# Kernel optimization log

Hardware: AMD Instinct MI355X
Metric: run time of the kernel (lower is better)

## Reference

```python
import jax, jax.numpy as jnp
import numpy as np

D_MODEL = 1024
D_STATE = 64
BATCH = 4
SEQ_L = 4096
LN_EPS = 1e-5


def setup_inputs() -> dict:
    key = jax.random.key(0)
    ks = jax.random.split(key, 8)
    u = jax.random.normal(ks[0], (BATCH, SEQ_L, D_MODEL), jnp.float32)
    # Parameters mirroring StateSpaceLayer._initialize_parameters
    A_log = jax.random.uniform(ks[1], (D_STATE,), jnp.float32, -2.0, -0.1)
    xav = float(np.sqrt(6.0 / (D_STATE + D_MODEL)))
    B = jax.random.uniform(ks[2], (D_STATE, D_MODEL), jnp.float32, -xav, xav) * 0.1
    C = jax.random.uniform(ks[3], (D_MODEL, D_STATE), jnp.float32, -xav, xav) * 0.1
    D = jnp.zeros((D_MODEL,), jnp.float32)
    delta = jax.random.uniform(ks[4], (D_MODEL,), jnp.float32, 0.001, 0.1)
    gamma = jnp.ones((D_MODEL,), jnp.float32)
    beta = jnp.zeros((D_MODEL,), jnp.float32)
    freq_align = jax.random.normal(ks[5], (D_MODEL,), jnp.float32)
    reward = jax.random.normal(ks[6], (D_MODEL,), jnp.float32)
    return dict(u=u, A_log=A_log, B=B, C=C, D=D, delta=delta,
                gamma=gamma, beta=beta, freq_align=freq_align, reward=reward)


def reference(u, A_log, B, C, D, delta, gamma, beta, freq_align, reward):
    b, L, d = u.shape
    A = -jnp.exp(A_log)                                   # [N]
    # --- convolution kernel: K[k] = C @ (A_bar[0])^k, A_bar[0] = exp(delta[0]*A) ---
    k_idx = jnp.arange(L, dtype=u.dtype)                  # [L]
    powers = jnp.exp(k_idx[:, None] * (delta[0] * A)[None, :])  # [L, N]
    K = jnp.einsum('ln,dn->ld', powers, C)                # [L, D]
    # --- FFT-based causal (circular, zero-padded) convolution ---
    fft_size = 1 << int(np.ceil(np.log2(2 * L)))
    u_fft = jnp.fft.fft(u, n=fft_size, axis=1)            # [B, F, D] complex
    K_fft = jnp.fft.fft(K, n=fft_size, axis=0)            # [F, D] complex
    y = jnp.fft.ifft(u_fft * K_fft[None], axis=1).real[:, :L, :]
    # --- D skip connection ---
    y = y + u * D
    # --- FFT-based learning signals: scale spectrum, add real 'reward' to every bin ---
    y_fft = jnp.fft.fft(y, axis=1)
    y = jnp.fft.ifft(y_fft * freq_align + reward, axis=1).real
    # --- LayerNorm (eval-mode dropout = identity) ---
    mean = y.mean(-1, keepdims=True)
    var = y.var(-1, keepdims=True)
    y = (y - mean) / jnp.sqrt(var + LN_EPS) * gamma + beta
    # --- final state update with mean timescale ---
    delta_mean = delta.mean()
    A_bar_s = jnp.exp(delta_mean * A)                     # [N]
    A_safe = A + 1e-8 * jnp.sign(A)
    B_bar = ((A_bar_s - 1.0) / A_safe)[:, None] * B       # [N, D]
    state = jnp.zeros((b, A.shape[0]), u.dtype)
    final_state = A_bar_s * state + jnp.einsum('nd,bd->bn', B_bar, u[:, -1, :])
    return (y, final_state)
```

## Files before the change

kernel.cpp:

```cpp
#include <hip/hip_runtime.h>
#include <math.h>

#define BATCH  4
#define SEQL   4096
#define DMODEL 1024
#define NSTATE 64
#define LN_EPS 1e-5f
#define TB     16

typedef unsigned short u16;
typedef float f32x2 __attribute__((ext_vector_type(2)));

__device__ __forceinline__ f32x2 fma2(f32x2 a, f32x2 b, f32x2 c) {
#if __has_builtin(__builtin_elementwise_fma)
    return __builtin_elementwise_fma(a, b, c);
#else
    f32x2 d; d.x = fmaf(a.x, b.x, c.x); d.y = fmaf(a.y, b.y, c.y); return d;
#endif
}

__device__ __forceinline__ u16 f2bf(float x) {
    unsigned int b = __float_as_uint(x);
    b += 0x7FFF + ((b >> 16) & 1);
    return (u16)(b >> 16);
}
__device__ __forceinline__ float bf2f(u16 h) {
    return __uint_as_float(((unsigned int)h) << 16);
}

__global__ __launch_bounds__(256) void k_local(const float* __restrict__ u,
                                               const float* __restrict__ A_log,
                                               const float* __restrict__ delta,
                                               u16* __restrict__ f,
                                               int NCH, int TCH) {
    __shared__ float r_lds[NSTATE];
    const int tid = threadIdx.x;
    const int w = tid >> 6, l = tid & 63;
    const int b   = blockIdx.x / (16 * NCH);
    const int rem = blockIdx.x % (16 * NCH);
    const int dt  = rem / NCH;
    const int j   = rem % NCH;
    const int n0  = w << 4;
    const int d   = (dt << 6) | l;

    if (tid < NSTATE) r_lds[tid] = expf(delta[0] * -expf(A_log[tid]));
    __syncthreads();

    f32x2 r2[8], s2[8];
#pragma unroll
    for (int p = 0; p < 8; ++p) {
        r2[p] = *(const f32x2*)&r_lds[n0 + 2 * p];
        s2[p] = (f32x2)(0.f, 0.f);
    }

    const float* ub = u + ((size_t)b * SEQL + (size_t)j * TCH) * DMODEL + d;
    for (int tb = 0; tb < TCH / TB; ++tb) {
        float ur[TB];
#pragma unroll
        for (int t = 0; t < TB; ++t)
            ur[t] = ub[(size_t)(tb * TB + t) * DMODEL];
#pragma unroll
        for (int q = 0; q < 4; ++q) {
            f32x2 sa = s2[2*q], sb = s2[2*q+1];
            const f32x2 ra = r2[2*q], rb = r2[2*q+1];
#pragma unroll
            for (int t = 0; t < TB; ++t) {
                f32x2 u2; u2.x = ur[t]; u2.y = ur[t];
                sa = fma2(ra, sa, u2);
                sb = fma2(rb, sb, u2);
            }
            s2[2*q] = sa; s2[2*q+1] = sb;
        }
    }
    u16* fb = f + (((size_t)b * NCH + j) * NSTATE + n0) * DMODEL + d;
#pragma unroll
    for (int p = 0; p < 8; ++p) {
        fb[(size_t)(2*p)     * DMODEL] = f2bf(s2[p].x);
        fb[(size_t)(2*p + 1) * DMODEL] = f2bf(s2[p].y);
    }
}

__global__ __launch_bounds__(256) void k_pass2(const float* __restrict__ A_log,
                                               const float* __restrict__ delta,
                                               u16* __restrict__ f,
                                               int NCH, int TCH) {
    const int tid = blockIdx.x * 256 + threadIdx.x;
    const int d = tid & (DMODEL - 1);
    const int n = (tid >> 10) & (NSTATE - 1);
    const int b = tid >> 16;
    const float A  = -expf(A_log[n]);
    const float rT = expf((float)TCH * delta[0] * A);
    float I = 0.f;
    u16* p = f + ((size_t)b * NCH * NSTATE + n) * DMODEL + d;
    const size_t stride = (size_t)NSTATE * DMODEL;
    for (int j = 0; j < NCH; ++j) {
        float tmp = bf2f(p[(size_t)j * stride]);
        p[(size_t)j * stride] = f2bf(I);
        I = fmaf(rT, I, tmp);
    }
}

__global__ __launch_bounds__(256) void k_replay(const float* __restrict__ u,
                                                const float* __restrict__ A_log,
                                                const float* __restrict__ C,
                                                const float* __restrict__ Dvec,
                                                const float* __restrict__ delta,
                                                const u16* __restrict__ I,
                                                const float* __restrict__ fal,
                                                const float* __restrict__ rw,
                                                float* __restrict__ z,
                                                int NCH, int TCH) {
    __shared__ float r_lds[NSTATE];
    __shared__ float part[4][TB][64];
    const int tid = threadIdx.x;
    const int w = tid >> 6, l = tid & 63;
    const int b   = blockIdx.x / (16 * NCH);
    const int rem = blockIdx.x % (16 * NCH);
    const int dt  = rem / NCH;
    const int j   = rem % NCH;
    const int n0  = w << 4;
    const int d   = (dt << 6) | l;

    if (tid < NSTATE) r_lds[tid] = expf(delta[0] * -expf(A_log[tid]));
    __syncthreads();

    const float fad = fal[d];
    f32x2 r2[8], c2[8], s2[8];
#pragma unroll
    for (int p = 0; p < 8; ++p)
        r2[p] = *(const f32x2*)&r_lds[n0 + 2 * p];
#pragma unroll
    for (int p = 0; p < 8; ++p) {
        c2[p].x = fad * C[(size_t)d * NSTATE + n0 + 2*p];
        c2[p].y = fad * C[(size_t)d * NSTATE + n0 + 2*p + 1];
    }
    const u16* Ib = I + (((size_t)b * NCH + j) * NSTATE + n0) * DMODEL + d;
#pragma unroll
    for (int p = 0; p < 8; ++p) {
        s2[p].x = bf2f(Ib[(size_t)(2*p)     * DMODEL]);
        s2[p].y = bf2f(Ib[(size_t)(2*p + 1) * DMODEL]);
    }

    const float Ddf = Dvec[d] * fad;
    const float rwd = rw[d];
    const float* ub = u + ((size_t)b * SEQL + (size_t)j * TCH) * DMODEL + d;
    float*       zb = z + ((size_t)b * SEQL + (size_t)j * TCH) * DMODEL + d;

    for (int tb = 0; tb < TCH / TB; ++tb) {
        float ur[TB];
        f32x2 zr2[TB];
#pragma unroll
        for (int t = 0; t < TB; ++t) {
            ur[t] = ub[(size_t)(tb * TB + t) * DMODEL];
            zr2[t] = (f32x2)(0.f, 0.f);
        }
#pragma unroll
        for (int q = 0; q < 4; ++q) {
            f32x2 sa = s2[2*q], sb = s2[2*q+1];
            const f32x2 ra = r2[2*q], rb = r2[2*q+1];
            const f32x2 ca = c2[2*q], cb = c2[2*q+1];
#pragma unroll
            for (int t = 0; t < TB; ++t) {
                f32x2 u2; u2.x = ur[t]; u2.y = ur[t];
                sa = fma2(ra, sa, u2);
                sb = fma2(rb, sb, u2);
                zr2[t] = fma2(ca, sa, zr2[t]);
                zr2[t] = fma2(cb, sb, zr2[t]);
            }
            s2[2*q] = sa; s2[2*q+1] = sb;
        }
#pragma unroll
        for (int t = 0; t < TB; ++t) {
            float v = zr2[t].x + zr2[t].y;
            if (w == 0) v = fmaf(Ddf, ur[t], v);
            part[w][t][l] = v;
        }
        __syncthreads();
#pragma unroll
        for (int k = 0; k < 4; ++k) {
            const int t = (w << 2) | k;
            float v = (part[0][t][l] + part[1][t][l]) +
                      (part[2][t][l] + part[3][t][l]);
            if (j == 0 && tb == 0 && t == 0) v += rwd;
            zb[(size_t)(tb * TB + t) * DMODEL] = v;
        }
        __syncthreads();
    }
}

__global__ __launch_bounds__(256) void k_ln(float* __restrict__ y,
                                            const float* __restrict__ gamma,
                                            const float* __restrict__ beta) {
    const int tid = threadIdx.x;
    float4* row = (float4*)(y + (size_t)blockIdx.x * DMODEL);
    float4 v = row[tid];
    float sum = v.x + v.y + v.z + v.w;
    float sq  = v.x*v.x + v.y*v.y + v.z*v.z + v.w*v.w;
#pragma unroll
    for (int off = 32; off > 0; off >>= 1) {
        sum += __shfl_down(sum, off, 64);
        sq  += __shfl_down(sq,  off, 64);
    }
    __shared__ float red[8];
    const int wave = tid >> 6, lane = tid & 63;
    if (lane == 0) { red[wave] = sum; red[4 + wave] = sq; }
    __syncthreads();
    sum = red[0] + red[1] + red[2] + red[3];
    sq  = red[4] + red[5] + red[6] + red[7];
    const float mean = sum * (1.f / DMODEL);
    const float var  = sq * (1.f / DMODEL) - mean * mean;
    const float inv  = 1.f / sqrtf(var + LN_EPS);
    const float4 g  = ((const float4*)gamma)[tid];
    const float4 bb = ((const float4*)beta)[tid];
    float4 o;
    o.x = (v.x - mean) * inv * g.x + bb.x;
    o.y = (v.y - mean) * inv * g.y + bb.y;
    o.z = (v.z - mean) * inv * g.z + bb.z;
    o.w = (v.w - mean) * inv * g.w + bb.w;
    row[tid] = o;
}

__global__ __launch_bounds__(256) void k_state(const float* __restrict__ u,
                                               const float* __restrict__ A_log,
                                               const float* __restrict__ B,
                                               const float* __restrict__ delta,
                                               float* __restrict__ out) {
    const int n = blockIdx.x & 63;
    const int b = blockIdx.x >> 6;
    const int tid = threadIdx.x;
    const float* ul = u + ((size_t)b * SEQL + (SEQL - 1)) * DMODEL;
    const float* Bn = B + (size_t)n * DMODEL;
    float dot = 0.f, dsum = 0.f;
    for (int dd = tid; dd < DMODEL; dd += 256) {
        dot = fmaf(Bn[dd], ul[dd], dot);
        dsum += delta[dd];
    }
#pragma unroll
    for (int off = 32; off > 0; off >>= 1) {
        dot  += __shfl_down(dot,  off, 64);
        dsum += __shfl_down(dsum, off, 64);
    }
    __shared__ float red[8];
    const int wave = tid >> 6, lane = tid & 63;
    if (lane == 0) { red[wave] = dot; red[4 + wave] = dsum; }
    __syncthreads();
    if (tid == 0) {
        dot  = red[0] + red[1] + red[2] + red[3];
        dsum = red[4] + red[5] + red[6] + red[7];
        const float dmean = dsum * (1.f / DMODEL);
        const float A = -expf(A_log[n]);
        const float Abar = expf(dmean * A);
        const float Asafe = A + (A >= 0.f ? 1e-8f : -1e-8f);
        out[blockIdx.x] = ((Abar - 1.f) / Asafe) * dot;
    }
}

extern "C" void kernel_launch(void* const* d_in, const int* in_sizes, int n_in,
                              void* d_out, int out_size, void* d_ws, size_t ws_size,
                              hipStream_t stream) {
    const float* u     = (const float*)d_in[0];
    const float* A_log = (const float*)d_in[1];
    const float* B     = (const float*)d_in[2];
    const float* C     = (const float*)d_in[3];
    const float* Dv    = (const float*)d_in[4];
    const float* delta = (const float*)d_in[5];
    const float* gamma = (const float*)d_in[6];
    const float* beta  = (const float*)d_in[7];
    const float* fal   = (const float*)d_in[8];
    const float* rw    = (const float*)d_in[9];

    float* y  = (float*)d_out;
    float* st = y + (size_t)BATCH * SEQL * DMODEL;
    u16* f    = (u16*)d_ws;

    int NCH = 32;
    while (NCH > 4 && (size_t)BATCH * NCH * NSTATE * DMODEL * sizeof(u16) > ws_size)
        NCH >>= 1;
    const int TCH = SEQL / NCH;
    const int nb = BATCH * 16 * NCH;

    hipLaunchKernelGGL(k_local, dim3(nb), dim3(256), 0, stream, u, A_log, delta, f, NCH, TCH);
    hipLaunchKernelGGL(k_pass2, dim3(BATCH * NSTATE * DMODEL / 256), dim3(256), 0, stream,
                       A_log, delta, f, NCH, TCH);
    hipLaunchKernelGGL(k_replay, dim3(nb), dim3(256), 0, stream,
                       u, A_log, C, Dv, delta, f, fal, rw, y, NCH, TCH);
    hipLaunchKernelGGL(k_ln, dim3(BATCH * SEQL), dim3(256), 0, stream, y, gamma, beta);
    hipLaunchKernelGGL(k_state, dim3(BATCH * NSTATE), dim3(256), 0, stream,
                       u, A_log, B, delta, st);
}
```

Measured before the change: 130.8 us.

## Store replay output as bf16 intermediate and double-buffer reduction LDS

```diff
diff --git a/kernel.cpp b/kernel.cpp
--- a/kernel.cpp
+++ b/kernel.cpp
@@ -100,6 +100,7 @@
     }
 }
 
+template <bool ZBF16>
 __global__ __launch_bounds__(256) void k_replay(const float* __restrict__ u,
                                                 const float* __restrict__ A_log,
                                                 const float* __restrict__ C,
@@ -108,10 +109,10 @@
                                                 const u16* __restrict__ I,
                                                 const float* __restrict__ fal,
                                                 const float* __restrict__ rw,
-                                                float* __restrict__ z,
+                                                void* __restrict__ zout,
                                                 int NCH, int TCH) {
     __shared__ float r_lds[NSTATE];
-    __shared__ float part[4][TB][64];
+    __shared__ float part[2][4][TB][64];
     const int tid = threadIdx.x;
     const int w = tid >> 6, l = tid & 63;
     const int b   = blockIdx.x / (16 * NCH);
@@ -144,9 +145,12 @@
     const float Ddf = Dvec[d] * fad;
     const float rwd = rw[d];
     const float* ub = u + ((size_t)b * SEQL + (size_t)j * TCH) * DMODEL + d;
-    float*       zb = z + ((size_t)b * SEQL + (size_t)j * TCH) * DMODEL + d;
+    const size_t zoff = ((size_t)b * SEQL + (size_t)j * TCH) * DMODEL + d;
+    u16*   zb16 = (u16*)zout + zoff;
+    float* zb32 = (float*)zout + zoff;
 
     for (int tb = 0; tb < TCH / TB; ++tb) {
+        const int pb = tb & 1;
         float ur[TB];
         f32x2 zr2[TB];
 #pragma unroll
@@ -173,27 +177,34 @@
         for (int t = 0; t < TB; ++t) {
             float v = zr2[t].x + zr2[t].y;
             if (w == 0) v = fmaf(Ddf, ur[t], v);
-            part[w][t][l] = v;
+            part[pb][w][t][l] = v;
         }
         __syncthreads();
 #pragma unroll
         for (int k = 0; k < 4; ++k) {
             const int t = (w << 2) | k;
-            float v = (part[0][t][l] + part[1][t][l]) +
-                      (part[2][t][l] + part[3][t][l]);
+            float v = (part[pb][0][t][l] + part[pb][1][t][l]) +
+                      (part[pb][2][t][l] + part[pb][3][t][l]);
             if (j == 0 && tb == 0 && t == 0) v += rwd;
-            zb[(size_t)(tb * TB + t) * DMODEL] = v;
-        }
-        __syncthreads();
-    }
-}
-
-__global__ __launch_bounds__(256) void k_ln(float* __restrict__ y,
+            if (ZBF16) zb16[(size_t)(tb * TB + t) * DMODEL] = f2bf(v);
+            else       zb32[(size_t)(tb * TB + t) * DMODEL] = v;
+        }
+    }
+}
+
+template <bool ZBF16>
+__global__ __launch_bounds__(256) void k_ln(const void* __restrict__ zin,
+                                            float* __restrict__ y,
                                             const float* __restrict__ gamma,
                                             const float* __restrict__ beta) {
     const int tid = threadIdx.x;
-    float4* row = (float4*)(y + (size_t)blockIdx.x * DMODEL);
-    float4 v = row[tid];
+    float4 v;
+    if (ZBF16) {
+        const ushort4 h = ((const ushort4*)((const u16*)zin + (size_t)blockIdx.x * DMODEL))[tid];
+        v.x = bf2f(h.x); v.y = bf2f(h.y); v.z = bf2f(h.z); v.w = bf2f(h.w);
+    } else {
+        v = ((const float4*)((const float*)zin + (size_t)blockIdx.x * DMODEL))[tid];
+    }
     float sum = v.x + v.y + v.z + v.w;
     float sq  = v.x*v.x + v.y*v.y + v.z*v.z + v.w*v.w;
 #pragma unroll
@@ -217,7 +228,7 @@
     o.y = (v.y - mean) * inv * g.y + bb.y;
     o.z = (v.z - mean) * inv * g.z + bb.z;
     o.w = (v.w - mean) * inv * g.w + bb.w;
-    row[tid] = o;
+    ((float4*)(y + (size_t)blockIdx.x * DMODEL))[tid] = o;
 }
 
 __global__ __launch_bounds__(256) void k_state(const float* __restrict__ u,
@@ -279,12 +290,25 @@
     const int TCH = SEQL / NCH;
     const int nb = BATCH * 16 * NCH;
 
+    const size_t f_bytes = (size_t)BATCH * NCH * NSTATE * DMODEL * sizeof(u16);
+    const size_t z_bytes = (size_t)BATCH * SEQL * DMODEL * sizeof(u16);
+    const bool zbf16 = (f_bytes + z_bytes) <= ws_size;
+    void* zbuf = zbf16 ? (void*)((char*)d_ws + f_bytes) : (void*)y;
+
     hipLaunchKernelGGL(k_local, dim3(nb), dim3(256), 0, stream, u, A_log, delta, f, NCH, TCH);
     hipLaunchKernelGGL(k_pass2, dim3(BATCH * NSTATE * DMODEL / 256), dim3(256), 0, stream,
                        A_log, delta, f, NCH, TCH);
-    hipLaunchKernelGGL(k_replay, dim3(nb), dim3(256), 0, stream,
-                       u, A_log, C, Dv, delta, f, fal, rw, y, NCH, TCH);
-    hipLaunchKernelGGL(k_ln, dim3(BATCH * SEQL), dim3(256), 0, stream, y, gamma, beta);
+    if (zbf16) {
+        hipLaunchKernelGGL((k_replay<true>), dim3(nb), dim3(256), 0, stream,
+                           u, A_log, C, Dv, delta, f, fal, rw, zbuf, NCH, TCH);
+        hipLaunchKernelGGL((k_ln<true>), dim3(BATCH * SEQL), dim3(256), 0, stream,
+                           zbuf, y, gamma, beta);
+    } else {
+        hipLaunchKernelGGL((k_replay<false>), dim3(nb), dim3(256), 0, stream,
+                           u, A_log, C, Dv, delta, f, fal, rw, zbuf, NCH, TCH);
+        hipLaunchKernelGGL((k_ln<false>), dim3(BATCH * SEQL), dim3(256), 0, stream,
+                           zbuf, y, gamma, beta);
+    }
     hipLaunchKernelGGL(k_state, dim3(BATCH * NSTATE), dim3(256), 0, stream,
                        u, A_log, B, delta, st);
 }
```

New measurement: 124.1 us. 1.05x faster.
